# Kernel optimization log

Hardware: AMD Instinct MI355X
Metric: run time of the kernel (lower is better)

Reference implementation:

```python
import jax, jax.numpy as jnp
import numpy as np

B, C, H, W, P, D, NH = 16, 3, 512, 512, 16, 128, 4
GH, GW = H // P, W // P
NP_ = GH * GW            # 1024 total patches
PD = C * P * P           # 768 patch dim
NV = NP_ // 4            # 256 visible tokens (mask_ratio = 0.75)
ENC_L, DEC_L = 6, 2
FF = 4 * D

def layer_norm(x, w, b, eps=1e-5):
    m = jnp.mean(x, -1, keepdims=True)
    v = jnp.mean((x - m) ** 2, -1, keepdims=True)
    return (x - m) * jax.lax.rsqrt(v + eps) * w + b

def mha(x, qkv_w, qkv_b, out_w, out_b):
    Bq, S, Dm = x.shape
    hd = Dm // NH
    q, k, v = jnp.split(x @ qkv_w.T + qkv_b, 3, axis=-1)
    sh = lambda t: t.reshape(Bq, S, NH, hd).transpose(0, 2, 1, 3)
    q, k, v = sh(q), sh(k), sh(v)
    scale = jnp.asarray(1.0 / np.sqrt(hd), x.dtype)
    att = jax.nn.softmax(jnp.einsum('bhqd,bhkd->bhqk', q, k) * scale, axis=-1)
    o = jnp.einsum('bhqk,bhkd->bhqd', att, v).transpose(0, 2, 1, 3).reshape(Bq, S, Dm)
    return o @ out_w.T + out_b

def stack(x, qkv_w, qkv_b, out_w, out_b, ln1_w, ln1_b, ff1_w, ff1_b, ff2_w, ff2_b, ln2_w, ln2_b):
    # post-norm nn.TransformerEncoderLayer, eval mode (dropout off), exact gelu
    for i in range(qkv_w.shape[0]):
        x = layer_norm(x + mha(x, qkv_w[i], qkv_b[i], out_w[i], out_b[i]), ln1_w[i], ln1_b[i])
        h = jax.nn.gelu(x @ ff1_w[i].T + ff1_b[i], approximate=False) @ ff2_w[i].T + ff2_b[i]
        x = layer_norm(x + h, ln2_w[i], ln2_b[i])
    return x

def setup_inputs():
    key = jax.random.key(0)
    ks = iter(jax.random.split(key, 64))
    f = lambda *s: jax.random.normal(next(ks), s, jnp.float32) * 0.02
    inp = {
        'x': jax.random.normal(next(ks), (B, C, H, W), jnp.float32),
        'vis_idx': jax.vmap(lambda k: jax.random.permutation(k, NP_))(jax.random.split(next(ks), B))[:, :NV].astype(jnp.int32),
        'w_patch': f(D, PD), 'b_patch': jnp.zeros((D,), jnp.float32),
        'mask_token': f(1, D), 'pos_embed': f(1, NP_, D),
        'w_recon': f(PD, D), 'b_recon': jnp.zeros((PD,), jnp.float32),
    }
    for pre, L in (('enc', ENC_L), ('dec', DEC_L)):
        inp[pre + '_qkv_w'] = f(L, 3 * D, D)
        inp[pre + '_qkv_b'] = jnp.zeros((L, 3 * D), jnp.float32)
        inp[pre + '_out_w'] = f(L, D, D)
        inp[pre + '_out_b'] = jnp.zeros((L, D), jnp.float32)
        inp[pre + '_ln1_w'] = jnp.ones((L, D), jnp.float32)
        inp[pre + '_ln1_b'] = jnp.zeros((L, D), jnp.float32)
        inp[pre + '_ff1_w'] = f(L, FF, D)
        inp[pre + '_ff1_b'] = jnp.zeros((L, FF), jnp.float32)
        inp[pre + '_ff2_w'] = f(L, D, FF)
        inp[pre + '_ff2_b'] = jnp.zeros((L, D), jnp.float32)
        inp[pre + '_ln2_w'] = jnp.ones((L, D), jnp.float32)
        inp[pre + '_ln2_b'] = jnp.zeros((L, D), jnp.float32)
    return inp

def reference(x, vis_idx, w_patch, b_patch, mask_token, pos_embed, w_recon, b_recon,
              enc_qkv_w, enc_qkv_b, enc_out_w, enc_out_b, enc_ln1_w, enc_ln1_b,
              enc_ff1_w, enc_ff1_b, enc_ff2_w, enc_ff2_b, enc_ln2_w, enc_ln2_b,
              dec_qkv_w, dec_qkv_b, dec_out_w, dec_out_b, dec_ln1_w, dec_ln1_b,
              dec_ff1_w, dec_ff1_b, dec_ff2_w, dec_ff2_b, dec_ln2_w, dec_ln2_b):
    # patchify: matches nn.Unfold(kernel=stride=P) channel-major patch layout
    patches = x.reshape(B, C, GH, P, GW, P).transpose(0, 2, 4, 1, 3, 5).reshape(B, NP_, PD)
    tok = patches @ w_patch.T + b_patch                    # [B, NP, D]
    bidx = jnp.arange(B)[:, None]
    vis = tok[bidx, vis_idx]                               # [B, NV, D] packed visible tokens
    enc = stack(vis, enc_qkv_w, enc_qkv_b, enc_out_w, enc_out_b, enc_ln1_w, enc_ln1_b,
                enc_ff1_w, enc_ff1_b, enc_ff2_w, enc_ff2_b, enc_ln2_w, enc_ln2_b)
    # mask_token everywhere, scatter encoded tokens back to their positions
    full = jnp.broadcast_to(mask_token, (B, NP_, D)).at[bidx, vis_idx].set(enc)
    full = full + pos_embed
    dec = stack(full, dec_qkv_w, dec_qkv_b, dec_out_w, dec_out_b, dec_ln1_w, dec_ln1_b,
                dec_ff1_w, dec_ff1_b, dec_ff2_w, dec_ff2_b, dec_ln2_w, dec_ln2_b)
    rec = dec @ w_recon.T + b_recon                        # [B, NP, PD]
    # unpatchify: [B,GH,GW,C,P,P] -> permute(0,3,1,4,2,5) -> [B,C,H,W]
    img = rec.reshape(B, GH, GW, C, P, P).transpose(0, 3, 1, 4, 2, 5).reshape(B, C, H, W)
    return img
```

## Files before the change

### kernel.cpp

```cpp
#include <hip/hip_runtime.h>
#include <math.h>

typedef unsigned short ushort_t;
typedef __attribute__((ext_vector_type(8))) short bf16x8;
typedef __attribute__((ext_vector_type(4))) float f32x4;
typedef __attribute__((ext_vector_type(16))) float f32x16;
typedef __attribute__((ext_vector_type(2))) unsigned uint2v;

__device__ __forceinline__ ushort_t f2bf(float f){
  union{float f; unsigned u;} v; v.f = f;
  unsigned r = v.u + 0x7FFFu + ((v.u >> 16) & 1u);
  return (ushort_t)(r >> 16);
}
__device__ __forceinline__ float bf2f(ushort_t h){
  union{unsigned u; float f;} v; v.u = ((unsigned)h) << 16; return v.f;
}
__device__ __forceinline__ float gelu_exact(float v){
  return 0.5f * v * (1.f + erff(v * 0.70710678118654752f));
}
#define GLD16(gp, lp) __builtin_amdgcn_global_load_lds( \
    (const __attribute__((address_space(1))) void*)(gp), \
    (__attribute__((address_space(3))) void*)(lp), 16, 0, 0)

static __device__ __forceinline__ f32x4 mfma16(bf16x8 a, bf16x8 b, f32x4 c){
  return __builtin_amdgcn_mfma_f32_16x16x32_bf16(a, b, c, 0, 0, 0);
}
static __device__ __forceinline__ f32x16 mfma32(bf16x8 a, bf16x8 b, f32x16 c){
  return __builtin_amdgcn_mfma_f32_32x32x16_bf16(a, b, c, 0, 0, 0);
}

template<int BT, int MI, int SRC, int EPI>
__global__ __launch_bounds__(256) void mfma_gemm(
    const ushort_t* __restrict__ A, const ushort_t* __restrict__ W,
    const float* __restrict__ bias, void* __restrict__ Cout,
    int M, int N, int K, ushort_t* __restrict__ vT, int slog, float qs)
{
  __shared__ ushort_t smem[BT*64 + BT*64];
  ushort_t* Al = smem;
  ushort_t* Wl = smem + BT*64;
  const int tid = threadIdx.x;
  const int lane = tid & 63, w = tid >> 6;
  const int wr = w >> 1, wc = w & 1;
  const int g = lane >> 4, lq = lane & 15;
  const int m0 = blockIdx.y * BT, n0 = blockIdx.x * BT;

  const f32x4 zf = {0.f, 0.f, 0.f, 0.f};
  f32x4 acc[MI][MI];
#pragma unroll
  for (int i = 0; i < MI; ++i)
#pragma unroll
    for (int j = 0; j < MI; ++j) acc[i][j] = zf;

  float bv[MI];
#pragma unroll
  for (int ni = 0; ni < MI; ++ni) bv[ni] = bias[n0 + wc*(BT/2) + ni*16 + lq];

  const int KT = K >> 6;
  for (int kt = 0; kt < KT; ++kt) {
    if (kt) __syncthreads();
    const int k0 = kt << 6;
#pragma unroll
    for (int i = 0; i < BT/32; ++i) {
      int chunk = i*256 + tid;
      int row = chunk >> 3, c = chunk & 7;
      int kk = k0 + ((c ^ (row & 7)) << 3);
      const ushort_t* src;
      if (SRC == 0) {
        src = A + (size_t)(m0 + row) * K + kk;
      } else {
        int gm = m0 + row;
        int bb = gm >> 10, pp = gm & 1023, gh = pp >> 5, gw = pp & 31;
        int ci = kk >> 8, rem = kk & 255, py = rem >> 4, px = rem & 15;
        src = A + ((size_t)((bb*3 + ci)*512 + gh*16 + py) * 512 + gw*16 + px);
      }
      GLD16(src, (char*)Al + chunk*16);
    }
#pragma unroll
    for (int i = 0; i < BT/32; ++i) {
      int chunk = i*256 + tid;
      int row = chunk >> 3, c = chunk & 7;
      int kk = k0 + ((c ^ (row & 7)) << 3);
      GLD16(W + (size_t)(n0 + row) * K + kk, (char*)Wl + chunk*16);
    }
    __syncthreads();
#pragma unroll
    for (int ks = 0; ks < 2; ++ks) {
      bf16x8 af[MI], bfr[MI];
#pragma unroll
      for (int mi = 0; mi < MI; ++mi) {
        int row = wr*(BT/2) + mi*16 + lq;
        int c = (ks*4 + g) ^ (row & 7);
        af[mi] = *(const bf16x8*)((const char*)Al + row*128 + c*16);
      }
#pragma unroll
      for (int ni = 0; ni < MI; ++ni) {
        int row = wc*(BT/2) + ni*16 + lq;
        int c = (ks*4 + g) ^ (row & 7);
        bfr[ni] = *(const bf16x8*)((const char*)Wl + row*128 + c*16);
      }
#pragma unroll
      for (int mi = 0; mi < MI; ++mi)
#pragma unroll
        for (int ni = 0; ni < MI; ++ni)
          acc[mi][ni] = mfma16(af[mi], bfr[ni], acc[mi][ni]);
    }
  }

  if (EPI == 3 && n0 >= 256) {
    const int Sm1 = (1 << slog) - 1;
#pragma unroll
    for (int mi = 0; mi < MI; ++mi) {
      int gm0 = m0 + wr*(BT/2) + mi*16 + g*4;
      int bb = gm0 >> slog, s0 = gm0 & Sm1;
#pragma unroll
      for (int ni = 0; ni < MI; ++ni) {
        int n = n0 + wc*(BT/2) + ni*16 + lq;
        int vcol = n - 256, hh = vcol >> 5, dd = vcol & 31;
        unsigned pw0 = ((unsigned)f2bf(acc[mi][ni][0] + bv[ni])) |
                       (((unsigned)f2bf(acc[mi][ni][1] + bv[ni])) << 16);
        unsigned pw1 = ((unsigned)f2bf(acc[mi][ni][2] + bv[ni])) |
                       (((unsigned)f2bf(acc[mi][ni][3] + bv[ni])) << 16);
        uint2 pk; pk.x = pw0; pk.y = pw1;
        *(uint2*)(vT + (((size_t)(bb*4 + hh)*32 + dd) << slog) + s0) = pk;
      }
    }
    return;
  }

  if (EPI == 2) {
    float* img = (float*)Cout;
#pragma unroll
    for (int mi = 0; mi < MI; ++mi) {
#pragma unroll
      for (int r = 0; r < 4; ++r) {
        int gm = m0 + wr*(BT/2) + mi*16 + g*4 + r;
        int bb = gm >> 10, pp = gm & 1023, gh = pp >> 5, gw = pp & 31;
#pragma unroll
        for (int ni = 0; ni < MI; ++ni) {
          int n = n0 + wc*(BT/2) + ni*16 + lq;
          int ci = n >> 8, rem = n & 255, py = rem >> 4, px = rem & 15;
          img[(size_t)((bb*3 + ci)*512 + gh*16 + py)*512 + gw*16 + px] =
              acc[mi][ni][r] + bv[ni];
        }
      }
    }
  } else {
    const float cs = (EPI == 3 && n0 < 128) ? qs : 1.0f;
    __syncthreads();
    constexpr int CPR = BT/8;
#pragma unroll
    for (int mi = 0; mi < MI; ++mi)
#pragma unroll
      for (int ni = 0; ni < MI; ++ni)
#pragma unroll
        for (int r = 0; r < 4; ++r) {
          int row = wr*(BT/2) + mi*16 + g*4 + r;
          int col = wc*(BT/2) + ni*16 + lq;
          float v = acc[mi][ni][r] + bv[ni];
          if (EPI == 3) v *= cs;
          int cc = (col >> 3) ^ (row & (CPR-1));
          smem[row*BT + cc*8 + (col & 7)] = f2bf(v);
        }
    __syncthreads();
    ushort_t* Co = (ushort_t*)Cout;
#pragma unroll
    for (int i = 0; i < BT*BT/2048; ++i) {
      int chunk = i*256 + tid;
      int row = chunk / CPR, cc = chunk % CPR;
      int c = cc ^ (row & (CPR-1));
      bf16x8 v = *(const bf16x8*)((const char*)smem + chunk*16);
      *(bf16x8*)(Co + (size_t)(m0+row)*N + n0 + c*8) = v;
    }
  }
}

template<int KK>
__global__ __launch_bounds__(256) void gemm_ln(
    const ushort_t* __restrict__ A, const ushort_t* __restrict__ W,
    const float* __restrict__ bias, ushort_t* __restrict__ X,
    const float* __restrict__ lnw, const float* __restrict__ lnb)
{
  __shared__ __align__(16) ushort_t Al[32*64];
  __shared__ __align__(16) ushort_t Wl[128*64];
  __shared__ float red[2][32][4];
  const int tid = threadIdx.x, lane = tid & 63, w = tid >> 6;
  const int g = lane >> 4, lq = lane & 15;
  const int m0 = blockIdx.x * 32;
  const f32x4 zf = {0.f,0.f,0.f,0.f};
  f32x4 acc[2][2] = {{zf,zf},{zf,zf}};

#pragma unroll
  for (int kt = 0; kt < KK/64; ++kt) {
    if (kt) __syncthreads();
    const int k0 = kt*64;
    { int row = tid >> 3, c = tid & 7;
      int kk = k0 + ((c ^ (row & 7)) << 3);
      GLD16(A + (size_t)(m0+row)*KK + kk, (char*)Al + tid*16); }
#pragma unroll
    for (int i = 0; i < 4; ++i) {
      int chunk = i*256 + tid, row = chunk >> 3, c = chunk & 7;
      int kk = k0 + ((c ^ (row & 7)) << 3);
      GLD16(W + (size_t)row*KK + kk, (char*)Wl + chunk*16);
    }
    __syncthreads();
#pragma unroll
    for (int ks = 0; ks < 2; ++ks) {
      bf16x8 af[2], bfr[2];
#pragma unroll
      for (int mi = 0; mi < 2; ++mi) {
        int row = mi*16 + lq, c = (ks*4 + g) ^ (row & 7);
        af[mi] = *(const bf16x8*)((const char*)Al + row*128 + c*16);
      }
#pragma unroll
      for (int ni = 0; ni < 2; ++ni) {
        int row = w*32 + ni*16 + lq, c = (ks*4 + g) ^ (row & 7);
        bfr[ni] = *(const bf16x8*)((const char*)Wl + row*128 + c*16);
      }
#pragma unroll
      for (int mi = 0; mi < 2; ++mi)
#pragma unroll
        for (int ni = 0; ni < 2; ++ni)
          acc[mi][ni] = mfma16(af[mi], bfr[ni], acc[mi][ni]);
    }
  }

  float bv[2], lwv[2], lbv[2];
#pragma unroll
  for (int ni = 0; ni < 2; ++ni) {
    int col = w*32 + ni*16 + lq;
    bv[ni] = bias[col]; lwv[ni] = lnw[col]; lbv[ni] = lnb[col];
  }
  float v[2][2][4];
#pragma unroll
  for (int mi = 0; mi < 2; ++mi)
#pragma unroll
    for (int r = 0; r < 4; ++r) {
      int row = m0 + mi*16 + g*4 + r;
#pragma unroll
      for (int ni = 0; ni < 2; ++ni) {
        int col = w*32 + ni*16 + lq;
        v[mi][ni][r] = acc[mi][ni][r] + bv[ni] + bf2f(X[(size_t)row*128 + col]);
      }
      float s = v[mi][0][r] + v[mi][1][r];
      float q = v[mi][0][r]*v[mi][0][r] + v[mi][1][r]*v[mi][1][r];
      s += __shfl_xor(s,1); s += __shfl_xor(s,2); s += __shfl_xor(s,4); s += __shfl_xor(s,8);
      q += __shfl_xor(q,1); q += __shfl_xor(q,2); q += __shfl_xor(q,4); q += __shfl_xor(q,8);
      if (lq == 0) { red[0][mi*16+g*4+r][w] = s; red[1][mi*16+g*4+r][w] = q; }
    }
  __syncthreads();
#pragma unroll
  for (int mi = 0; mi < 2; ++mi)
#pragma unroll
    for (int r = 0; r < 4; ++r) {
      int rl = mi*16 + g*4 + r;
      float s = red[0][rl][0]+red[0][rl][1]+red[0][rl][2]+red[0][rl][3];
      float q = red[1][rl][0]+red[1][rl][1]+red[1][rl][2]+red[1][rl][3];
      float mean = s * 0.0078125f;
      float var = q * 0.0078125f - mean*mean;
      float rstd = rsqrtf(var + 1e-5f);
#pragma unroll
      for (int ni = 0; ni < 2; ++ni) {
        int col = w*32 + ni*16 + lq;
        X[(size_t)(m0+rl)*128 + col] = f2bf((v[mi][ni][r]-mean)*rstd*lwv[ni] + lbv[ni]);
      }
    }
}

__global__ __launch_bounds__(256) void ffn_ln(
    ushort_t* __restrict__ X,
    const ushort_t* __restrict__ W1, const float* __restrict__ b1,
    const ushort_t* __restrict__ W2, const float* __restrict__ b2,
    const float* __restrict__ lnw, const float* __restrict__ lnb)
{
  __shared__ __align__(16) ushort_t Xl[2*32*64];
  __shared__ __align__(16) ushort_t Hl[8*32*64];
  __shared__ __align__(16) ushort_t Wl[128*64];
  __shared__ float red[2][32][4];
  const int tid = threadIdx.x, lane = tid & 63, w = tid >> 6;
  const int g = lane >> 4, lq = lane & 15;
  const int m0 = blockIdx.x * 32;
  const f32x4 zf = {0.f,0.f,0.f,0.f};

#pragma unroll
  for (int i = 0; i < 2; ++i) {
    int chunk = i*256 + tid;
    int kt = chunk >> 8, r8 = chunk & 255, row = r8 >> 3, c = r8 & 7;
    int kk = kt*64 + ((c ^ (row & 7)) << 3);
    GLD16(X + (size_t)(m0+row)*128 + kk, (char*)Xl + chunk*16);
  }

#pragma unroll
  for (int hp = 0; hp < 4; ++hp) {
    f32x4 acc1[2][2] = {{zf,zf},{zf,zf}};
#pragma unroll
    for (int kt = 0; kt < 2; ++kt) {
      __syncthreads();
#pragma unroll
      for (int i = 0; i < 4; ++i) {
        int chunk = i*256 + tid, row = chunk >> 3, c = chunk & 7;
        int kk = kt*64 + ((c ^ (row & 7)) << 3);
        GLD16(W1 + (size_t)(hp*128 + row)*128 + kk, (char*)Wl + chunk*16);
      }
      __syncthreads();
#pragma unroll
      for (int ks = 0; ks < 2; ++ks) {
        bf16x8 af[2], bfr[2];
#pragma unroll
        for (int mi = 0; mi < 2; ++mi) {
          int row = mi*16 + lq, c = (ks*4 + g) ^ (row & 7);
          af[mi] = *(const bf16x8*)((const char*)Xl + kt*4096 + row*128 + c*16);
        }
#pragma unroll
        for (int ni = 0; ni < 2; ++ni) {
          int row = w*32 + ni*16 + lq, c = (ks*4 + g) ^ (row & 7);
          bfr[ni] = *(const bf16x8*)((const char*)Wl + row*128 + c*16);
        }
#pragma unroll
        for (int mi = 0; mi < 2; ++mi)
#pragma unroll
          for (int ni = 0; ni < 2; ++ni)
            acc1[mi][ni] = mfma16(af[mi], bfr[ni], acc1[mi][ni]);
      }
    }
#pragma unroll
    for (int ni = 0; ni < 2; ++ni) {
      int hid = hp*128 + w*32 + ni*16 + lq;
      float bb = b1[hid];
      int hkt = hid >> 6, hc = (hid & 63) >> 3, he = hid & 7;
#pragma unroll
      for (int mi = 0; mi < 2; ++mi)
#pragma unroll
        for (int r = 0; r < 4; ++r) {
          int mrow = mi*16 + g*4 + r;
          float hv = gelu_exact(acc1[mi][ni][r] + bb);
          *(ushort_t*)((char*)Hl + hkt*4096 + mrow*128 +
                       ((hc ^ (mrow & 7)) << 4) + he*2) = f2bf(hv);
        }
    }
  }

  f32x4 acc2[2][2] = {{zf,zf},{zf,zf}};
#pragma unroll
  for (int kt = 0; kt < 8; ++kt) {
    __syncthreads();
#pragma unroll
    for (int i = 0; i < 4; ++i) {
      int chunk = i*256 + tid, row = chunk >> 3, c = chunk & 7;
      int kk = kt*64 + ((c ^ (row & 7)) << 3);
      GLD16(W2 + (size_t)row*512 + kk, (char*)Wl + chunk*16);
    }
    __syncthreads();
#pragma unroll
    for (int ks = 0; ks < 2; ++ks) {
      bf16x8 af[2], bfr[2];
#pragma unroll
      for (int mi = 0; mi < 2; ++mi) {
        int row = mi*16 + lq, c = (ks*4 + g) ^ (row & 7);
        af[mi] = *(const bf16x8*)((const char*)Hl + kt*4096 + row*128 + c*16);
      }
#pragma unroll
      for (int ni = 0; ni < 2; ++ni) {
        int row = w*32 + ni*16 + lq, c = (ks*4 + g) ^ (row & 7);
        bfr[ni] = *(const bf16x8*)((const char*)Wl + row*128 + c*16);
      }
#pragma unroll
      for (int mi = 0; mi < 2; ++mi)
#pragma unroll
        for (int ni = 0; ni < 2; ++ni)
          acc2[mi][ni] = mfma16(af[mi], bfr[ni], acc2[mi][ni]);
    }
  }

  float bv[2], lwv[2], lbv[2];
#pragma unroll
  for (int ni = 0; ni < 2; ++ni) {
    int col = w*32 + ni*16 + lq;
    bv[ni] = b2[col]; lwv[ni] = lnw[col]; lbv[ni] = lnb[col];
  }
  float v[2][2][4];
#pragma unroll
  for (int mi = 0; mi < 2; ++mi)
#pragma unroll
    for (int r = 0; r < 4; ++r) {
      int row = m0 + mi*16 + g*4 + r;
#pragma unroll
      for (int ni = 0; ni < 2; ++ni) {
        int col = w*32 + ni*16 + lq;
        v[mi][ni][r] = acc2[mi][ni][r] + bv[ni] + bf2f(X[(size_t)row*128 + col]);
      }
      float s = v[mi][0][r] + v[mi][1][r];
      float q = v[mi][0][r]*v[mi][0][r] + v[mi][1][r]*v[mi][1][r];
      s += __shfl_xor(s,1); s += __shfl_xor(s,2); s += __shfl_xor(s,4); s += __shfl_xor(s,8);
      q += __shfl_xor(q,1); q += __shfl_xor(q,2); q += __shfl_xor(q,4); q += __shfl_xor(q,8);
      if (lq == 0) { red[0][mi*16+g*4+r][w] = s; red[1][mi*16+g*4+r][w] = q; }
    }
  __syncthreads();
#pragma unroll
  for (int mi = 0; mi < 2; ++mi)
#pragma unroll
    for (int r = 0; r < 4; ++r) {
      int rl = mi*16 + g*4 + r;
      float s = red[0][rl][0]+red[0][rl][1]+red[0][rl][2]+red[0][rl][3];
      float q = red[1][rl][0]+red[1][rl][1]+red[1][rl][2]+red[1][rl][3];
      float mean = s * 0.0078125f;
      float var = q * 0.0078125f - mean*mean;
      float rstd = rsqrtf(var + 1e-5f);
#pragma unroll
      for (int ni = 0; ni < 2; ++ni) {
        int col = w*32 + ni*16 + lq;
        X[(size_t)(m0+rl)*128 + col] = f2bf((v[mi][ni][r]-mean)*rstd*lwv[ni] + lbv[ni]);
      }
    }
}

template<int S, int JS>
__global__ __launch_bounds__(256) void attn32(
    const ushort_t* __restrict__ qkv, const ushort_t* __restrict__ vTg,
    ushort_t* __restrict__ o)
{
  constexpr int LDSB = (JS == 1) ? 16384 : 32768;
  __shared__ __align__(16) char smem[LDSB];
  const int tid = threadIdx.x, lane = tid & 63, w = tid >> 6;
  const int hi = lane >> 5, lq = lane & 31;
  int lin = blockIdx.x;
  int nid = (lin & 7) * 64 + (lin >> 3);
  int bx = nid & 7, bh = nid >> 3;
  int h = bh & 3, b = bh >> 2;
  const int q0 = (JS == 1) ? (bx*128 + w*32) : (bx*32);

  bf16x8 bq0 = *(const bf16x8*)(qkv + (size_t)(b*S + q0 + lq)*384 + h*32 + hi*8);
  bf16x8 bq1 = *(const bf16x8*)(qkv + (size_t)(b*S + q0 + lq)*384 + h*32 + 16 + hi*8);

  f32x16 O;
#pragma unroll
  for (int i = 0; i < 16; ++i) O[i] = 0.f;
  const f32x16 z16 = O;
  float l = 0.f;

  auto stageK = [&](char* Kb, int j0, int ci){
    int k = ci >> 2, cp = ci & 3, c = cp ^ (k & 3);
    GLD16(qkv + (size_t)(b*S + j0 + k)*384 + 128 + h*32 + c*8, Kb + ci*16);
  };
  auto stageV = [&](char* Vb, int j0, int ci){
    int d = ci >> 3, cp = ci & 7, c = cp ^ (d & 7);
    GLD16(vTg + (size_t)(bh*32 + d)*S + j0 + c*8, Vb + ci*16);
  };

  auto sm_pack = [&](const f32x16& stv, unsigned* wd){
    float p[16];
#pragma unroll
    for (int r = 0; r < 16; ++r) { p[r] = __expf(stv[r]); l += p[r]; }
#pragma unroll
    for (int i = 0; i < 8; ++i) {
      unsigned u0 = __float_as_uint(p[2*i])   + 0x8000u;
      unsigned u1 = __float_as_uint(p[2*i+1]) + 0x8000u;
      wd[i] = (u0 >> 16) | (u1 & 0xFFFF0000u);
    }
  };
  auto pvstep = [&](unsigned* wd, const char* Vb, int mt){
    uint2v s02 = __builtin_amdgcn_permlane32_swap(wd[0], wd[2], false, false);
    uint2v s13 = __builtin_amdgcn_permlane32_swap(wd[1], wd[3], false, false);
    uint2v s46 = __builtin_amdgcn_permlane32_swap(wd[4], wd[6], false, false);
    uint2v s57 = __builtin_amdgcn_permlane32_swap(wd[5], wd[7], false, false);
    union { unsigned u[4]; bf16x8 v; } pa0, pa1;
    pa0.u[0] = s02[0]; pa0.u[1] = s13[0]; pa0.u[2] = s02[1]; pa0.u[3] = s13[1];
    pa1.u[0] = s46[0]; pa1.u[1] = s57[0]; pa1.u[2] = s46[1]; pa1.u[3] = s57[1];
    int d = lq;
    bf16x8 v0 = *(const bf16x8*)(Vb + d*128 + (((mt*4 + hi)     ^ (d & 7)) << 4));
    bf16x8 v1 = *(const bf16x8*)(Vb + d*128 + (((mt*4 + 2 + hi) ^ (d & 7)) << 4));
    O = mfma32(pa0.v, v0, O);
    O = mfma32(pa1.v, v1, O);
  };
  auto computeTile = [&](const char* Kb, const char* Vb){
    const int k0 = lq, k1 = 32 + lq;
    bf16x8 a00 = *(const bf16x8*)(Kb + k0*64 + (((hi)     ^ (k0 & 3)) << 4));
    bf16x8 a01 = *(const bf16x8*)(Kb + k0*64 + (((2 + hi) ^ (k0 & 3)) << 4));
    f32x16 st0 = mfma32(a00, bq0, z16);
    st0 = mfma32(a01, bq1, st0);
    bf16x8 a10 = *(const bf16x8*)(Kb + k1*64 + (((hi)     ^ (k1 & 3)) << 4));
    bf16x8 a11 = *(const bf16x8*)(Kb + k1*64 + (((2 + hi) ^ (k1 & 3)) << 4));
    f32x16 st1 = mfma32(a10, bq0, z16);
    st1 = mfma32(a11, bq1, st1);
    unsigned wd0[8], wd1[8];
    sm_pack(st0, wd0);
    sm_pack(st1, wd1);
    pvstep(wd0, Vb, 0);
    pvstep(wd1, Vb, 1);
  };

  if (JS == 4) {
    char* Kb = smem + w*8192;
    char* Vb = Kb + 4096;
    const int j0 = w*64;
#pragma unroll
    for (int i = 0; i < 4; ++i) stageK(Kb, j0, i*64 + lane);
#pragma unroll
    for (int i = 0; i < 4; ++i) stageV(Vb, j0, i*64 + lane);
    __syncthreads();
    computeTile(Kb, Vb);
    float lw = l + __shfl_xor(l, 32);
    __syncthreads();
    float* F = (float*)smem;
#pragma unroll
    for (int r = 0; r < 16; ++r) F[(w*16 + r)*64 + lane] = O[r];
    if (hi == 0) F[4096 + w*32 + lq] = lw;
    __syncthreads();
    if (w == 0) {
      float lt = F[4096 + lq] + F[4096 + 32 + lq] + F[4096 + 64 + lq] + F[4096 + 96 + lq];
      float linv = 1.f / lt;
#pragma unroll
      for (int r = 0; r < 16; ++r) {
        float s = F[r*64 + lane] + F[(16 + r)*64 + lane] +
                  F[(32 + r)*64 + lane] + F[(48 + r)*64 + lane];
        int qr = (r & 3) + 8*(r >> 2) + 4*hi;
        float li = __shfl(linv, qr);
        o[(size_t)(b*S + q0 + qr)*128 + h*32 + lq] = f2bf(s*li);
      }
    }
  } else {
    char* K0 = smem, *V0 = smem + 4096, *K1 = smem + 8192, *V1 = smem + 12288;
    stageK(K0, 0, tid);
    stageV(V0, 0, tid);
    const int NT = S/64;
    for (int t = 0; t < NT; ++t) {
      __syncthreads();
      if (t + 1 < NT) {
        char* Kb = (t & 1) ? K0 : K1;
        char* Vb = (t & 1) ? V0 : V1;
        stageK(Kb, (t + 1)*64, tid);
        stageV(Vb, (t + 1)*64, tid);
      }
      computeTile((t & 1) ? K1 : K0, (t & 1) ? V1 : V0);
    }
    float ltot = l + __shfl_xor(l, 32);
    float linv = 1.f / ltot;
#pragma unroll
    for (int r = 0; r < 16; ++r) {
      int qr = (r & 3) + 8*(r >> 2) + 4*hi;
      float li = __shfl(linv, qr);
      o[(size_t)(b*S + q0 + qr)*128 + h*32 + lq] = f2bf(O[r]*li);
    }
  }
}

struct CastArgs {
  const float* src[11];
  ushort_t* dst[11];
  int start[11];
};
__global__ __launch_bounds__(256) void cast_all(CastArgs a, int total8){
  int i = blockIdx.x*256 + threadIdx.x;
  if (i >= total8) return;
  int s = 0;
#pragma unroll
  for (int k = 1; k < 11; ++k) if (i >= a.start[k]) s = k;
  int off = (i - a.start[s]) * 8;
  const float* sp = a.src[s] + off;
  float4 f0 = *(const float4*)sp;
  float4 f1 = *(const float4*)(sp + 4);
  bf16x8 r;
  r[0]=(short)f2bf(f0.x); r[1]=(short)f2bf(f0.y); r[2]=(short)f2bf(f0.z); r[3]=(short)f2bf(f0.w);
  r[4]=(short)f2bf(f1.x); r[5]=(short)f2bf(f1.y); r[6]=(short)f2bf(f1.z); r[7]=(short)f2bf(f1.w);
  *(bf16x8*)(a.dst[s] + off) = r;
}

__global__ __launch_bounds__(256) void gather_k(const ushort_t* __restrict__ tok,
    const int* __restrict__ vis, ushort_t* __restrict__ xe){
  int i = blockIdx.x*256 + threadIdx.x;
  int r = i >> 4, e = (i & 15)*8;
  int b = r >> 8;
  int p = vis[r];
  *(bf16x8*)(xe + (size_t)r*128 + e) = *(const bf16x8*)(tok + ((size_t)b*1024 + p)*128 + e);
}

__global__ __launch_bounds__(256) void fill_k(const float* __restrict__ mask_tok,
    const float* __restrict__ pos, ushort_t* __restrict__ full){
  int i = blockIdx.x*256 + threadIdx.x;
  int off0 = i*8;
  int d = off0 & 127;
  int p = (off0 >> 7) & 1023;
  float4 m0 = *(const float4*)(mask_tok + d);
  float4 m1 = *(const float4*)(mask_tok + d + 4);
  const float* pp = pos + (size_t)p*128 + d;
  float4 p0 = *(const float4*)pp, p1 = *(const float4*)(pp + 4);
  bf16x8 r;
  r[0]=(short)f2bf(m0.x+p0.x); r[1]=(short)f2bf(m0.y+p0.y);
  r[2]=(short)f2bf(m0.z+p0.z); r[3]=(short)f2bf(m0.w+p0.w);
  r[4]=(short)f2bf(m1.x+p1.x); r[5]=(short)f2bf(m1.y+p1.y);
  r[6]=(short)f2bf(m1.z+p1.z); r[7]=(short)f2bf(m1.w+p1.w);
  *(bf16x8*)(full + off0) = r;
}

__global__ __launch_bounds__(256) void scatter_k(const ushort_t* __restrict__ enc,
    const int* __restrict__ vis, const float* __restrict__ pos, ushort_t* __restrict__ full){
  int i = blockIdx.x*256 + threadIdx.x;
  int r = i >> 4, e = (i & 15)*8;
  int b = r >> 8;
  int p = vis[r];
  bf16x8 ev = *(const bf16x8*)(enc + (size_t)r*128 + e);
  const float* pp = pos + (size_t)p*128 + e;
  float4 p0 = *(const float4*)pp, p1 = *(const float4*)(pp + 4);
  bf16x8 out;
  out[0]=(short)f2bf(bf2f((ushort_t)ev[0]) + p0.x);
  out[1]=(short)f2bf(bf2f((ushort_t)ev[1]) + p0.y);
  out[2]=(short)f2bf(bf2f((ushort_t)ev[2]) + p0.z);
  out[3]=(short)f2bf(bf2f((ushort_t)ev[3]) + p0.w);
  out[4]=(short)f2bf(bf2f((ushort_t)ev[4]) + p1.x);
  out[5]=(short)f2bf(bf2f((ushort_t)ev[5]) + p1.y);
  out[6]=(short)f2bf(bf2f((ushort_t)ev[6]) + p1.z);
  out[7]=(short)f2bf(bf2f((ushort_t)ev[7]) + p1.w);
  *(bf16x8*)(full + ((size_t)b*1024 + p)*128 + e) = out;
}

extern "C" void kernel_launch(void* const* d_in, const int* in_sizes, int n_in,
                              void* d_out, int out_size, void* d_ws, size_t ws_size,
                              hipStream_t stream)
{
  const float* x        = (const float*)d_in[0];
  const int*   vis      = (const int*)d_in[1];
  const float* b_patch  = (const float*)d_in[3];
  const float* mask_tok = (const float*)d_in[4];
  const float* pos      = (const float*)d_in[5];
  const float* b_recon  = (const float*)d_in[7];
  float* out = (float*)d_out;
  const float QS = 0.17677669529663687f;

  ushort_t* ws    = (ushort_t*)d_ws;
  ushort_t* tok   = ws;
  ushort_t* xe    = tok  + 2097152;
  ushort_t* qkvb  = xe   + 524288;
  ushort_t* obuf  = qkvb + 8388608;
  ushort_t* tbuf  = obuf + 2097152;
  ushort_t* xbf   = tbuf + 2097152;
  ushort_t* wbf   = xbf  + 12582912;

  ushort_t* w_qkv_e = wbf;
  ushort_t* w_out_e = w_qkv_e + 294912;
  ushort_t* w_ff1_e = w_out_e + 98304;
  ushort_t* w_ff2_e = w_ff1_e + 393216;
  ushort_t* w_qkv_d = w_ff2_e + 393216;
  ushort_t* w_out_d = w_qkv_d + 98304;
  ushort_t* w_ff1_d = w_out_d + 32768;
  ushort_t* w_ff2_d = w_ff1_d + 131072;
  ushort_t* w_pat   = w_ff2_d + 131072;
  ushort_t* w_rec   = w_pat   + 98304;
  ushort_t* vT      = w_rec   + 98304;

  CastArgs ca;
  const float* srcs[11] = {x, (const float*)d_in[8], (const float*)d_in[10],
                           (const float*)d_in[14], (const float*)d_in[16],
                           (const float*)d_in[20], (const float*)d_in[22],
                           (const float*)d_in[26], (const float*)d_in[28],
                           (const float*)d_in[2], (const float*)d_in[6]};
  ushort_t* dsts[11] = {xbf, w_qkv_e, w_out_e, w_ff1_e, w_ff2_e,
                        w_qkv_d, w_out_d, w_ff1_d, w_ff2_d, w_pat, w_rec};
  int sizes[11] = {12582912, 294912, 98304, 393216, 393216,
                   98304, 32768, 131072, 131072, 98304, 98304};
  int acc8 = 0;
  for (int k = 0; k < 11; ++k){ ca.src[k]=srcs[k]; ca.dst[k]=dsts[k]; ca.start[k]=acc8; acc8 += sizes[k]/8; }
  cast_all<<<dim3((acc8 + 255)/256), 256, 0, stream>>>(ca, acc8);

  mfma_gemm<64,2,1,0><<<dim3(2,256), 256, 0, stream>>>(xbf, w_pat, b_patch, tok, 16384, 128, 768, nullptr, 0, 1.f);
  gather_k<<<dim3(256), 256, 0, stream>>>(tok, vis, xe);

  for (int L = 0; L < 6; ++L) {
    const float* qb  = (const float*)d_in[9]  + L*384;
    const float* ob  = (const float*)d_in[11] + L*128;
    const float* l1w = (const float*)d_in[12] + L*128;
    const float* l1b = (const float*)d_in[13] + L*128;
    const float* f1b = (const float*)d_in[15] + L*512;
    const float* f2b = (const float*)d_in[17] + L*128;
    const float* l2w = (const float*)d_in[18] + L*128;
    const float* l2b = (const float*)d_in[19] + L*128;
    mfma_gemm<64,2,0,3><<<dim3(6,64), 256, 0, stream>>>(xe, w_qkv_e + L*49152, qb, qkvb, 4096, 384, 128, vT, 8, QS);
    attn32<256,4><<<dim3(512), 256, 0, stream>>>(qkvb, vT, obuf);
    gemm_ln<128><<<dim3(128), 256, 0, stream>>>(obuf, w_out_e + L*16384, ob, xe, l1w, l1b);
    ffn_ln<<<dim3(128), 256, 0, stream>>>(xe, w_ff1_e + L*65536, f1b, w_ff2_e + L*65536, f2b, l2w, l2b);
  }

  fill_k<<<dim3(1024), 256, 0, stream>>>(mask_tok, pos, tok);
  scatter_k<<<dim3(256), 256, 0, stream>>>(xe, vis, pos, tok);

  for (int L = 0; L < 2; ++L) {
    const float* qb  = (const float*)d_in[21] + L*384;
    const float* ob  = (const float*)d_in[23] + L*128;
    const float* l1w = (const float*)d_in[24] + L*128;
    const float* l1b = (const float*)d_in[25] + L*128;
    const float* f1b = (const float*)d_in[27] + L*512;
    const float* f2b = (const float*)d_in[29] + L*128;
    const float* l2w = (const float*)d_in[30] + L*128;
    const float* l2b = (const float*)d_in[31] + L*128;
    mfma_gemm<128,4,0,3><<<dim3(3,128), 256, 0, stream>>>(tok, w_qkv_d + L*49152, qb, qkvb, 16384, 384, 128, vT, 10, QS);
    attn32<1024,1><<<dim3(512), 256, 0, stream>>>(qkvb, vT, obuf);
    gemm_ln<128><<<dim3(512), 256, 0, stream>>>(obuf, w_out_d + L*16384, ob, tok, l1w, l1b);
    ffn_ln<<<dim3(512), 256, 0, stream>>>(tok, w_ff1_d + L*65536, f1b, w_ff2_d + L*65536, f2b, l2w, l2b);
  }

  mfma_gemm<128,4,0,2><<<dim3(6,128), 256, 0, stream>>>(tok, w_rec, b_recon, out, 16384, 768, 128, nullptr, 0, 1.f);
}
```

Baseline: 400.1 us.

## Fuse out-proj, LN1, FFN, LN2 and next-layer QKV into one mega kernel

Merges the out-projection+LayerNorm kernel and the FFN+LayerNorm kernel into a single per-row-tile kernel. It also computes the next layer's QKV projection in the epilogue, so the standalone QKV GEMM runs only once before each stack. Weights are read directly from global memory into registers instead of being staged through LDS. This removes kernel launches, intermediate activation round-trips and several barriers. In exchange it uses smaller row tiles (16 rows in the encoder), more registers and uncached repeated weight reads per block.

```diff
diff --git a/kernel.cpp b/kernel.cpp
--- a/kernel.cpp
+++ b/kernel.cpp
@@ -174,243 +174,266 @@
   }
 }
 
-template<int KK>
-__global__ __launch_bounds__(256) void gemm_ln(
-    const ushort_t* __restrict__ A, const ushort_t* __restrict__ W,
-    const float* __restrict__ bias, ushort_t* __restrict__ X,
-    const float* __restrict__ lnw, const float* __restrict__ lnb)
+template<int MI2, int QKV>
+__global__ __launch_bounds__(256) void mega_mlp(
+    const ushort_t* __restrict__ Ao, const ushort_t* __restrict__ Wo,
+    const float* __restrict__ bo, ushort_t* __restrict__ X,
+    const float* __restrict__ l1w, const float* __restrict__ l1b,
+    const ushort_t* __restrict__ W1, const float* __restrict__ b1,
+    const ushort_t* __restrict__ W2, const float* __restrict__ b2,
+    const float* __restrict__ l2w, const float* __restrict__ l2b,
+    const ushort_t* __restrict__ Wq, const float* __restrict__ bq,
+    ushort_t* __restrict__ qkvb, ushort_t* __restrict__ vT,
+    int slog, float qs)
 {
-  __shared__ __align__(16) ushort_t Al[32*64];
-  __shared__ __align__(16) ushort_t Wl[128*64];
-  __shared__ float red[2][32][4];
+  constexpr int BM = MI2 * 16;
+  constexpr int TB = BM * 128;
+  __shared__ __align__(16) ushort_t Xl[2*BM*64];
+  __shared__ __align__(16) ushort_t Hl[8*BM*64];
+  __shared__ float red[2][BM][4];
   const int tid = threadIdx.x, lane = tid & 63, w = tid >> 6;
   const int g = lane >> 4, lq = lane & 15;
-  const int m0 = blockIdx.x * 32;
+  const int m0 = blockIdx.x * BM;
   const f32x4 zf = {0.f,0.f,0.f,0.f};
-  f32x4 acc[2][2] = {{zf,zf},{zf,zf}};
-
-#pragma unroll
-  for (int kt = 0; kt < KK/64; ++kt) {
-    if (kt) __syncthreads();
-    const int k0 = kt*64;
-    { int row = tid >> 3, c = tid & 7;
-      int kk = k0 + ((c ^ (row & 7)) << 3);
-      GLD16(A + (size_t)(m0+row)*KK + kk, (char*)Al + tid*16); }
-#pragma unroll
-    for (int i = 0; i < 4; ++i) {
-      int chunk = i*256 + tid, row = chunk >> 3, c = chunk & 7;
-      int kk = k0 + ((c ^ (row & 7)) << 3);
-      GLD16(W + (size_t)row*KK + kk, (char*)Wl + chunk*16);
-    }
-    __syncthreads();
-#pragma unroll
-    for (int ks = 0; ks < 2; ++ks) {
-      bf16x8 af[2], bfr[2];
-#pragma unroll
-      for (int mi = 0; mi < 2; ++mi) {
-        int row = mi*16 + lq, c = (ks*4 + g) ^ (row & 7);
-        af[mi] = *(const bf16x8*)((const char*)Al + row*128 + c*16);
-      }
-#pragma unroll
-      for (int ni = 0; ni < 2; ++ni) {
-        int row = w*32 + ni*16 + lq, c = (ks*4 + g) ^ (row & 7);
-        bfr[ni] = *(const bf16x8*)((const char*)Wl + row*128 + c*16);
-      }
-#pragma unroll
-      for (int mi = 0; mi < 2; ++mi)
+
+  f32x4 acc[MI2][2];
+#pragma unroll
+  for (int mi = 0; mi < MI2; ++mi) { acc[mi][0] = zf; acc[mi][1] = zf; }
+  {
+    bf16x8 a[MI2][4], b[2][4];
+#pragma unroll
+    for (int mi = 0; mi < MI2; ++mi)
+#pragma unroll
+      for (int kf = 0; kf < 4; ++kf)
+        a[mi][kf] = *(const bf16x8*)(Ao + (size_t)(m0 + mi*16 + lq)*128 + kf*32 + g*8);
+#pragma unroll
+    for (int ni = 0; ni < 2; ++ni)
+#pragma unroll
+      for (int kf = 0; kf < 4; ++kf)
+        b[ni][kf] = *(const bf16x8*)(Wo + (size_t)(w*32 + ni*16 + lq)*128 + kf*32 + g*8);
+#pragma unroll
+    for (int kf = 0; kf < 4; ++kf)
+#pragma unroll
+      for (int mi = 0; mi < MI2; ++mi)
 #pragma unroll
         for (int ni = 0; ni < 2; ++ni)
-          acc[mi][ni] = mfma16(af[mi], bfr[ni], acc[mi][ni]);
-    }
-  }
-
-  float bv[2], lwv[2], lbv[2];
-#pragma unroll
-  for (int ni = 0; ni < 2; ++ni) {
-    int col = w*32 + ni*16 + lq;
-    bv[ni] = bias[col]; lwv[ni] = lnw[col]; lbv[ni] = lnb[col];
-  }
-  float v[2][2][4];
-#pragma unroll
-  for (int mi = 0; mi < 2; ++mi)
-#pragma unroll
-    for (int r = 0; r < 4; ++r) {
-      int row = m0 + mi*16 + g*4 + r;
-#pragma unroll
-      for (int ni = 0; ni < 2; ++ni) {
-        int col = w*32 + ni*16 + lq;
-        v[mi][ni][r] = acc[mi][ni][r] + bv[ni] + bf2f(X[(size_t)row*128 + col]);
-      }
-      float s = v[mi][0][r] + v[mi][1][r];
-      float q = v[mi][0][r]*v[mi][0][r] + v[mi][1][r]*v[mi][1][r];
-      s += __shfl_xor(s,1); s += __shfl_xor(s,2); s += __shfl_xor(s,4); s += __shfl_xor(s,8);
-      q += __shfl_xor(q,1); q += __shfl_xor(q,2); q += __shfl_xor(q,4); q += __shfl_xor(q,8);
-      if (lq == 0) { red[0][mi*16+g*4+r][w] = s; red[1][mi*16+g*4+r][w] = q; }
-    }
+          acc[mi][ni] = mfma16(a[mi][kf], b[ni][kf], acc[mi][ni]);
+  }
+
+  float xp[MI2][2][4];
+  {
+    float bv[2], lwv[2], lbv[2];
+#pragma unroll
+    for (int ni = 0; ni < 2; ++ni) {
+      int col = w*32 + ni*16 + lq;
+      bv[ni] = bo[col]; lwv[ni] = l1w[col]; lbv[ni] = l1b[col];
+    }
+#pragma unroll
+    for (int mi = 0; mi < MI2; ++mi)
+#pragma unroll
+      for (int r = 0; r < 4; ++r) {
+        int row = m0 + mi*16 + g*4 + r;
+#pragma unroll
+        for (int ni = 0; ni < 2; ++ni) {
+          int col = w*32 + ni*16 + lq;
+          xp[mi][ni][r] = acc[mi][ni][r] + bv[ni] + bf2f(X[(size_t)row*128 + col]);
+        }
+        float s = xp[mi][0][r] + xp[mi][1][r];
+        float q = xp[mi][0][r]*xp[mi][0][r] + xp[mi][1][r]*xp[mi][1][r];
+        s += __shfl_xor(s,1); s += __shfl_xor(s,2); s += __shfl_xor(s,4); s += __shfl_xor(s,8);
+        q += __shfl_xor(q,1); q += __shfl_xor(q,2); q += __shfl_xor(q,4); q += __shfl_xor(q,8);
+        if (lq == 0) { red[0][mi*16+g*4+r][w] = s; red[1][mi*16+g*4+r][w] = q; }
+      }
+    __syncthreads();
+#pragma unroll
+    for (int mi = 0; mi < MI2; ++mi)
+#pragma unroll
+      for (int r = 0; r < 4; ++r) {
+        int rl = mi*16 + g*4 + r;
+        float s = red[0][rl][0]+red[0][rl][1]+red[0][rl][2]+red[0][rl][3];
+        float q = red[1][rl][0]+red[1][rl][1]+red[1][rl][2]+red[1][rl][3];
+        float mean = s * 0.0078125f;
+        float var = q * 0.0078125f - mean*mean;
+        float rstd = rsqrtf(var + 1e-5f);
+#pragma unroll
+        for (int ni = 0; ni < 2; ++ni) {
+          int col = w*32 + ni*16 + lq;
+          float val = (xp[mi][ni][r]-mean)*rstd*lwv[ni] + lbv[ni];
+          xp[mi][ni][r] = val;
+          ushort_t hv = f2bf(val);
+          X[(size_t)(m0+rl)*128 + col] = hv;
+          int kt = col >> 6, hc = (col & 63) >> 3, he = col & 7;
+          *(ushort_t*)((char*)Xl + kt*TB + rl*128 + ((hc ^ (rl & 7)) << 4) + he*2) = hv;
+        }
+      }
+  }
   __syncthreads();
-#pragma unroll
-  for (int mi = 0; mi < 2; ++mi)
-#pragma unroll
-    for (int r = 0; r < 4; ++r) {
-      int rl = mi*16 + g*4 + r;
-      float s = red[0][rl][0]+red[0][rl][1]+red[0][rl][2]+red[0][rl][3];
-      float q = red[1][rl][0]+red[1][rl][1]+red[1][rl][2]+red[1][rl][3];
-      float mean = s * 0.0078125f;
-      float var = q * 0.0078125f - mean*mean;
-      float rstd = rsqrtf(var + 1e-5f);
-#pragma unroll
-      for (int ni = 0; ni < 2; ++ni) {
-        int col = w*32 + ni*16 + lq;
-        X[(size_t)(m0+rl)*128 + col] = f2bf((v[mi][ni][r]-mean)*rstd*lwv[ni] + lbv[ni]);
-      }
-    }
-}
-
-__global__ __launch_bounds__(256) void ffn_ln(
-    ushort_t* __restrict__ X,
-    const ushort_t* __restrict__ W1, const float* __restrict__ b1,
-    const ushort_t* __restrict__ W2, const float* __restrict__ b2,
-    const float* __restrict__ lnw, const float* __restrict__ lnb)
-{
-  __shared__ __align__(16) ushort_t Xl[2*32*64];
-  __shared__ __align__(16) ushort_t Hl[8*32*64];
-  __shared__ __align__(16) ushort_t Wl[128*64];
-  __shared__ float red[2][32][4];
-  const int tid = threadIdx.x, lane = tid & 63, w = tid >> 6;
-  const int g = lane >> 4, lq = lane & 15;
-  const int m0 = blockIdx.x * 32;
-  const f32x4 zf = {0.f,0.f,0.f,0.f};
-
-#pragma unroll
-  for (int i = 0; i < 2; ++i) {
-    int chunk = i*256 + tid;
-    int kt = chunk >> 8, r8 = chunk & 255, row = r8 >> 3, c = r8 & 7;
-    int kk = kt*64 + ((c ^ (row & 7)) << 3);
-    GLD16(X + (size_t)(m0+row)*128 + kk, (char*)Xl + chunk*16);
-  }
-
+
+  bf16x8 a2[MI2][4];
+#pragma unroll
+  for (int mi = 0; mi < MI2; ++mi)
+#pragma unroll
+    for (int kf = 0; kf < 4; ++kf) {
+      int kt = kf >> 1, ks = kf & 1, row = mi*16 + lq;
+      int c = (ks*4 + g) ^ (row & 7);
+      a2[mi][kf] = *(const bf16x8*)((const char*)Xl + kt*TB + row*128 + c*16);
+    }
 #pragma unroll
   for (int hp = 0; hp < 4; ++hp) {
-    f32x4 acc1[2][2] = {{zf,zf},{zf,zf}};
-#pragma unroll
-    for (int kt = 0; kt < 2; ++kt) {
-      __syncthreads();
-#pragma unroll
-      for (int i = 0; i < 4; ++i) {
-        int chunk = i*256 + tid, row = chunk >> 3, c = chunk & 7;
-        int kk = kt*64 + ((c ^ (row & 7)) << 3);
-        GLD16(W1 + (size_t)(hp*128 + row)*128 + kk, (char*)Wl + chunk*16);
-      }
-      __syncthreads();
-#pragma unroll
-      for (int ks = 0; ks < 2; ++ks) {
-        bf16x8 af[2], bfr[2];
-#pragma unroll
-        for (int mi = 0; mi < 2; ++mi) {
-          int row = mi*16 + lq, c = (ks*4 + g) ^ (row & 7);
-          af[mi] = *(const bf16x8*)((const char*)Xl + kt*4096 + row*128 + c*16);
-        }
-#pragma unroll
-        for (int ni = 0; ni < 2; ++ni) {
-          int row = w*32 + ni*16 + lq, c = (ks*4 + g) ^ (row & 7);
-          bfr[ni] = *(const bf16x8*)((const char*)Wl + row*128 + c*16);
-        }
-#pragma unroll
-        for (int mi = 0; mi < 2; ++mi)
-#pragma unroll
-          for (int ni = 0; ni < 2; ++ni)
-            acc1[mi][ni] = mfma16(af[mi], bfr[ni], acc1[mi][ni]);
-      }
-    }
+    f32x4 acc1[MI2][2];
+#pragma unroll
+    for (int mi = 0; mi < MI2; ++mi) { acc1[mi][0] = zf; acc1[mi][1] = zf; }
+    bf16x8 b1f[2][4];
+#pragma unroll
+    for (int ni = 0; ni < 2; ++ni)
+#pragma unroll
+      for (int kf = 0; kf < 4; ++kf)
+        b1f[ni][kf] = *(const bf16x8*)(W1 + (size_t)(hp*128 + w*32 + ni*16 + lq)*128 + kf*32 + g*8);
+#pragma unroll
+    for (int kf = 0; kf < 4; ++kf)
+#pragma unroll
+      for (int mi = 0; mi < MI2; ++mi)
+#pragma unroll
+        for (int ni = 0; ni < 2; ++ni)
+          acc1[mi][ni] = mfma16(a2[mi][kf], b1f[ni][kf], acc1[mi][ni]);
 #pragma unroll
     for (int ni = 0; ni < 2; ++ni) {
       int hid = hp*128 + w*32 + ni*16 + lq;
       float bb = b1[hid];
       int hkt = hid >> 6, hc = (hid & 63) >> 3, he = hid & 7;
 #pragma unroll
-      for (int mi = 0; mi < 2; ++mi)
+      for (int mi = 0; mi < MI2; ++mi)
 #pragma unroll
         for (int r = 0; r < 4; ++r) {
           int mrow = mi*16 + g*4 + r;
           float hv = gelu_exact(acc1[mi][ni][r] + bb);
-          *(ushort_t*)((char*)Hl + hkt*4096 + mrow*128 +
-                       ((hc ^ (mrow & 7)) << 4) + he*2) = f2bf(hv);
+          *(ushort_t*)((char*)Hl + hkt*TB + mrow*128 + ((hc ^ (mrow & 7)) << 4) + he*2) = f2bf(hv);
         }
     }
   }
-
-  f32x4 acc2[2][2] = {{zf,zf},{zf,zf}};
-#pragma unroll
-  for (int kt = 0; kt < 8; ++kt) {
-    __syncthreads();
-#pragma unroll
-    for (int i = 0; i < 4; ++i) {
-      int chunk = i*256 + tid, row = chunk >> 3, c = chunk & 7;
-      int kk = kt*64 + ((c ^ (row & 7)) << 3);
-      GLD16(W2 + (size_t)row*512 + kk, (char*)Wl + chunk*16);
-    }
-    __syncthreads();
-#pragma unroll
-    for (int ks = 0; ks < 2; ++ks) {
-      bf16x8 af[2], bfr[2];
-#pragma unroll
-      for (int mi = 0; mi < 2; ++mi) {
-        int row = mi*16 + lq, c = (ks*4 + g) ^ (row & 7);
-        af[mi] = *(const bf16x8*)((const char*)Hl + kt*4096 + row*128 + c*16);
-      }
-#pragma unroll
-      for (int ni = 0; ni < 2; ++ni) {
-        int row = w*32 + ni*16 + lq, c = (ks*4 + g) ^ (row & 7);
-        bfr[ni] = *(const bf16x8*)((const char*)Wl + row*128 + c*16);
-      }
-#pragma unroll
-      for (int mi = 0; mi < 2; ++mi)
+  __syncthreads();
+
+  f32x4 acc2[MI2][2];
+#pragma unroll
+  for (int mi = 0; mi < MI2; ++mi) { acc2[mi][0] = zf; acc2[mi][1] = zf; }
+#pragma unroll
+  for (int kf = 0; kf < 16; ++kf) {
+    int kt = kf >> 1, ks = kf & 1;
+    bf16x8 af[MI2], bfr[2];
+#pragma unroll
+    for (int mi = 0; mi < MI2; ++mi) {
+      int row = mi*16 + lq, c = (ks*4 + g) ^ (row & 7);
+      af[mi] = *(const bf16x8*)((const char*)Hl + kt*TB + row*128 + c*16);
+    }
+#pragma unroll
+    for (int ni = 0; ni < 2; ++ni)
+      bfr[ni] = *(const bf16x8*)(W2 + (size_t)(w*32 + ni*16 + lq)*512 + kf*32 + g*8);
+#pragma unroll
+    for (int mi = 0; mi < MI2; ++mi)
+#pragma unroll
+      for (int ni = 0; ni < 2; ++ni)
+        acc2[mi][ni] = mfma16(af[mi], bfr[ni], acc2[mi][ni]);
+  }
+
+  {
+    float bv[2], lwv[2], lbv[2];
+#pragma unroll
+    for (int ni = 0; ni < 2; ++ni) {
+      int col = w*32 + ni*16 + lq;
+      bv[ni] = b2[col]; lwv[ni] = l2w[col]; lbv[ni] = l2b[col];
+    }
+#pragma unroll
+    for (int mi = 0; mi < MI2; ++mi)
+#pragma unroll
+      for (int r = 0; r < 4; ++r) {
 #pragma unroll
         for (int ni = 0; ni < 2; ++ni)
-          acc2[mi][ni] = mfma16(af[mi], bfr[ni], acc2[mi][ni]);
-    }
-  }
-
-  float bv[2], lwv[2], lbv[2];
-#pragma unroll
-  for (int ni = 0; ni < 2; ++ni) {
-    int col = w*32 + ni*16 + lq;
-    bv[ni] = b2[col]; lwv[ni] = lnw[col]; lbv[ni] = lnb[col];
-  }
-  float v[2][2][4];
-#pragma unroll
-  for (int mi = 0; mi < 2; ++mi)
-#pragma unroll
-    for (int r = 0; r < 4; ++r) {
-      int row = m0 + mi*16 + g*4 + r;
-#pragma unroll
-      for (int ni = 0; ni < 2; ++ni) {
-        int col = w*32 + ni*16 + lq;
-        v[mi][ni][r] = acc2[mi][ni][r] + bv[ni] + bf2f(X[(size_t)row*128 + col]);
-      }
-      float s = v[mi][0][r] + v[mi][1][r];
-      float q = v[mi][0][r]*v[mi][0][r] + v[mi][1][r]*v[mi][1][r];
-      s += __shfl_xor(s,1); s += __shfl_xor(s,2); s += __shfl_xor(s,4); s += __shfl_xor(s,8);
-      q += __shfl_xor(q,1); q += __shfl_xor(q,2); q += __shfl_xor(q,4); q += __shfl_xor(q,8);
-      if (lq == 0) { red[0][mi*16+g*4+r][w] = s; red[1][mi*16+g*4+r][w] = q; }
-    }
-  __syncthreads();
-#pragma unroll
-  for (int mi = 0; mi < 2; ++mi)
-#pragma unroll
-    for (int r = 0; r < 4; ++r) {
-      int rl = mi*16 + g*4 + r;
-      float s = red[0][rl][0]+red[0][rl][1]+red[0][rl][2]+red[0][rl][3];
-      float q = red[1][rl][0]+red[1][rl][1]+red[1][rl][2]+red[1][rl][3];
-      float mean = s * 0.0078125f;
-      float var = q * 0.0078125f - mean*mean;
-      float rstd = rsqrtf(var + 1e-5f);
-#pragma unroll
-      for (int ni = 0; ni < 2; ++ni) {
-        int col = w*32 + ni*16 + lq;
-        X[(size_t)(m0+rl)*128 + col] = f2bf((v[mi][ni][r]-mean)*rstd*lwv[ni] + lbv[ni]);
-      }
-    }
+          xp[mi][ni][r] = acc2[mi][ni][r] + bv[ni] + xp[mi][ni][r];
+        float s = xp[mi][0][r] + xp[mi][1][r];
+        float q = xp[mi][0][r]*xp[mi][0][r] + xp[mi][1][r]*xp[mi][1][r];
+        s += __shfl_xor(s,1); s += __shfl_xor(s,2); s += __shfl_xor(s,4); s += __shfl_xor(s,8);
+        q += __shfl_xor(q,1); q += __shfl_xor(q,2); q += __shfl_xor(q,4); q += __shfl_xor(q,8);
+        if (lq == 0) { red[0][mi*16+g*4+r][w] = s; red[1][mi*16+g*4+r][w] = q; }
+      }
+    __syncthreads();
+#pragma unroll
+    for (int mi = 0; mi < MI2; ++mi)
+#pragma unroll
+      for (int r = 0; r < 4; ++r) {
+        int rl = mi*16 + g*4 + r;
+        float s = red[0][rl][0]+red[0][rl][1]+red[0][rl][2]+red[0][rl][3];
+        float q = red[1][rl][0]+red[1][rl][1]+red[1][rl][2]+red[1][rl][3];
+        float mean = s * 0.0078125f;
+        float var = q * 0.0078125f - mean*mean;
+        float rstd = rsqrtf(var + 1e-5f);
+#pragma unroll
+        for (int ni = 0; ni < 2; ++ni) {
+          int col = w*32 + ni*16 + lq;
+          float val = (xp[mi][ni][r]-mean)*rstd*lwv[ni] + lbv[ni];
+          ushort_t hv = f2bf(val);
+          X[(size_t)(m0+rl)*128 + col] = hv;
+          if (QKV) {
+            int kt = col >> 6, hc = (col & 63) >> 3, he = col & 7;
+            *(ushort_t*)((char*)Xl + kt*TB + rl*128 + ((hc ^ (rl & 7)) << 4) + he*2) = hv;
+          }
+        }
+      }
+  }
+
+  if (QKV) {
+    __syncthreads();
+    bf16x8 a3[MI2][4];
+#pragma unroll
+    for (int mi = 0; mi < MI2; ++mi)
+#pragma unroll
+      for (int kf = 0; kf < 4; ++kf) {
+        int kt = kf >> 1, ks = kf & 1, row = mi*16 + lq;
+        int c = (ks*4 + g) ^ (row & 7);
+        a3[mi][kf] = *(const bf16x8*)((const char*)Xl + kt*TB + row*128 + c*16);
+      }
+    const int Sm1 = (1 << slog) - 1;
+#pragma unroll
+    for (int ni = 0; ni < 6; ++ni) {
+      int nb = w*96 + ni*16;
+      int col = nb + lq;
+      f32x4 aq[MI2];
+#pragma unroll
+      for (int mi = 0; mi < MI2; ++mi) aq[mi] = zf;
+      bf16x8 bq8[4];
+#pragma unroll
+      for (int kf = 0; kf < 4; ++kf)
+        bq8[kf] = *(const bf16x8*)(Wq + (size_t)col*128 + kf*32 + g*8);
+#pragma unroll
+      for (int kf = 0; kf < 4; ++kf)
+#pragma unroll
+        for (int mi = 0; mi < MI2; ++mi)
+          aq[mi] = mfma16(a3[mi][kf], bq8[kf], aq[mi]);
+      float bias = bq[col];
+      if (col < 256) {
+        float sc = (col < 128) ? qs : 1.f;
+#pragma unroll
+        for (int mi = 0; mi < MI2; ++mi)
+#pragma unroll
+          for (int r = 0; r < 4; ++r) {
+            int row = m0 + mi*16 + g*4 + r;
+            qkvb[(size_t)row*384 + col] = f2bf((aq[mi][r] + bias)*sc);
+          }
+      } else {
+        int vcol = col - 256, hh = vcol >> 5, dd = vcol & 31;
+#pragma unroll
+        for (int mi = 0; mi < MI2; ++mi) {
+          int gm0 = m0 + mi*16 + g*4;
+          int bb = gm0 >> slog, s0 = gm0 & Sm1;
+          unsigned pw0 = ((unsigned)f2bf(aq[mi][0] + bias)) |
+                         (((unsigned)f2bf(aq[mi][1] + bias)) << 16);
+          unsigned pw1 = ((unsigned)f2bf(aq[mi][2] + bias)) |
+                         (((unsigned)f2bf(aq[mi][3] + bias)) << 16);
+          uint2 pk; pk.x = pw0; pk.y = pw1;
+          *(uint2*)(vT + (((size_t)(bb*4 + hh)*32 + dd) << slog) + s0) = pk;
+        }
+      }
+    }
+  }
 }
 
 template<int S, int JS>
@@ -663,8 +686,8 @@
   mfma_gemm<64,2,1,0><<<dim3(2,256), 256, 0, stream>>>(xbf, w_pat, b_patch, tok, 16384, 128, 768, nullptr, 0, 1.f);
   gather_k<<<dim3(256), 256, 0, stream>>>(tok, vis, xe);
 
+  mfma_gemm<64,2,0,3><<<dim3(6,64), 256, 0, stream>>>(xe, w_qkv_e, (const float*)d_in[9], qkvb, 4096, 384, 128, vT, 8, QS);
   for (int L = 0; L < 6; ++L) {
-    const float* qb  = (const float*)d_in[9]  + L*384;
     const float* ob  = (const float*)d_in[11] + L*128;
     const float* l1w = (const float*)d_in[12] + L*128;
     const float* l1b = (const float*)d_in[13] + L*128;
@@ -672,17 +695,23 @@
     const float* f2b = (const float*)d_in[17] + L*128;
     const float* l2w = (const float*)d_in[18] + L*128;
     const float* l2b = (const float*)d_in[19] + L*128;
-    mfma_gemm<64,2,0,3><<<dim3(6,64), 256, 0, stream>>>(xe, w_qkv_e + L*49152, qb, qkvb, 4096, 384, 128, vT, 8, QS);
     attn32<256,4><<<dim3(512), 256, 0, stream>>>(qkvb, vT, obuf);
-    gemm_ln<128><<<dim3(128), 256, 0, stream>>>(obuf, w_out_e + L*16384, ob, xe, l1w, l1b);
-    ffn_ln<<<dim3(128), 256, 0, stream>>>(xe, w_ff1_e + L*65536, f1b, w_ff2_e + L*65536, f2b, l2w, l2b);
+    if (L < 5) {
+      mega_mlp<1,1><<<dim3(256), 256, 0, stream>>>(obuf, w_out_e + L*16384, ob, xe,
+          l1w, l1b, w_ff1_e + L*65536, f1b, w_ff2_e + L*65536, f2b, l2w, l2b,
+          w_qkv_e + (L+1)*49152, (const float*)d_in[9] + (L+1)*384, qkvb, vT, 8, QS);
+    } else {
+      mega_mlp<1,0><<<dim3(256), 256, 0, stream>>>(obuf, w_out_e + L*16384, ob, xe,
+          l1w, l1b, w_ff1_e + L*65536, f1b, w_ff2_e + L*65536, f2b, l2w, l2b,
+          w_qkv_e, (const float*)d_in[9], qkvb, vT, 8, QS);
+    }
   }
 
   fill_k<<<dim3(1024), 256, 0, stream>>>(mask_tok, pos, tok);
   scatter_k<<<dim3(256), 256, 0, stream>>>(xe, vis, pos, tok);
 
+  mfma_gemm<128,4,0,3><<<dim3(3,128), 256, 0, stream>>>(tok, w_qkv_d, (const float*)d_in[21], qkvb, 16384, 384, 128, vT, 10, QS);
   for (int L = 0; L < 2; ++L) {
-    const float* qb  = (const float*)d_in[21] + L*384;
     const float* ob  = (const float*)d_in[23] + L*128;
     const float* l1w = (const float*)d_in[24] + L*128;
     const float* l1b = (const float*)d_in[25] + L*128;
@@ -690,10 +719,16 @@
     const float* f2b = (const float*)d_in[29] + L*128;
     const float* l2w = (const float*)d_in[30] + L*128;
     const float* l2b = (const float*)d_in[31] + L*128;
-    mfma_gemm<128,4,0,3><<<dim3(3,128), 256, 0, stream>>>(tok, w_qkv_d + L*49152, qb, qkvb, 16384, 384, 128, vT, 10, QS);
     attn32<1024,1><<<dim3(512), 256, 0, stream>>>(qkvb, vT, obuf);
-    gemm_ln<128><<<dim3(512), 256, 0, stream>>>(obuf, w_out_d + L*16384, ob, tok, l1w, l1b);
-    ffn_ln<<<dim3(512), 256, 0, stream>>>(tok, w_ff1_d + L*65536, f1b, w_ff2_d + L*65536, f2b, l2w, l2b);
+    if (L < 1) {
+      mega_mlp<2,1><<<dim3(512), 256, 0, stream>>>(obuf, w_out_d + L*16384, ob, tok,
+          l1w, l1b, w_ff1_d + L*65536, f1b, w_ff2_d + L*65536, f2b, l2w, l2b,
+          w_qkv_d + 49152, (const float*)d_in[21] + 384, qkvb, vT, 10, QS);
+    } else {
+      mega_mlp<2,0><<<dim3(512), 256, 0, stream>>>(obuf, w_out_d + L*16384, ob, tok,
+          l1w, l1b, w_ff1_d + L*65536, f1b, w_ff2_d + L*65536, f2b, l2w, l2b,
+          w_qkv_d, (const float*)d_in[21], qkvb, vT, 10, QS);
+    }
   }
 
   mfma_gemm<128,4,0,2><<<dim3(6,128), 256, 0, stream>>>(tok, w_rec, b_recon, out, 16384, 768, 128, nullptr, 0, 1.f);
```

Measured after the change: 341.1 us. -14.7%, faster.
